# Kernel optimization log

Hardware: AMD Instinct MI355X
Metric: run time of the kernel (lower is better)

The kernel has to match this reference:

```python
import jax, jax.numpy as jnp
import numpy as np

D_MODEL = 192
D_STATE = 16
D_INNER = 384          # expand * d_model
DT_RANK = 12           # ceil(d_model / 16)
K = 4                  # 4 scan directions
B_, H_, W_ = 4, 64, 64
EPS = 1e-6


def setup_inputs() -> dict:
    key = jax.random.key(0)
    ks = jax.random.split(key, 7)
    x = jax.random.normal(ks[0], (B_, H_, W_, D_MODEL), jnp.float32)
    in_proj_weight = jax.random.normal(ks[1], (2 * D_INNER, D_MODEL), jnp.float32) * (D_MODEL ** -0.5)
    out_proj_weight = jax.random.normal(ks[2], (D_MODEL, D_INNER), jnp.float32) * (D_INNER ** -0.5)
    x_proj_weight = jax.random.normal(ks[3], (K, DT_RANK + 2 * D_STATE, D_INNER), jnp.float32) * 0.02
    dt_projs_weight = jax.random.normal(ks[4], (K, D_INNER, DT_RANK), jnp.float32) * (DT_RANK ** -0.5)
    # dt_init: bias = inv_softplus(dt), dt ~ loguniform[1e-3, 1e-1]
    dt = jnp.exp(jax.random.uniform(ks[5], (K, D_INNER)) * (np.log(0.1) - np.log(0.001)) + np.log(0.001))
    dt = jnp.clip(dt, 1e-4, None)
    dt_projs_bias = dt + jnp.log(-jnp.expm1(-dt))
    # A_log_init: log(1..N) repeated over K*d_inner rows
    A_logs = jnp.log(jnp.tile(jnp.arange(1, D_STATE + 1, dtype=jnp.float32)[None, :], (K * D_INNER, 1)))
    Ds = jnp.ones((K * D_INNER,), jnp.float32)
    out_norm_weight = jnp.ones((D_INNER,), jnp.float32)
    out_norm_bias = jnp.zeros((D_INNER,), jnp.float32)
    return dict(x=x, in_proj_weight=in_proj_weight, out_proj_weight=out_proj_weight,
                x_proj_weight=x_proj_weight, dt_projs_weight=dt_projs_weight,
                dt_projs_bias=dt_projs_bias, A_logs=A_logs, Ds=Ds,
                out_norm_weight=out_norm_weight, out_norm_bias=out_norm_bias)


def _selective_scan(u, delta, A, Bs, Cs, Ds, delta_bias):
    """u, delta: (B, K*D, L); A: (K*D, N); Bs, Cs: (B, K, N, L) (grouped); Ds: (K*D,)."""
    Bb, KD, L = u.shape
    N = A.shape[1]
    D = KD // K
    delta = jax.nn.softplus(delta + delta_bias[None, :, None])
    u_k = u.reshape(Bb, K, D, L)
    d_k = delta.reshape(Bb, K, D, L)
    A_k = A.reshape(K, D, N)

    def step(h, inp):
        dt, ut, bt, ct = inp              # dt, ut: (B,K,D); bt, ct: (B,K,N)
        dA = jnp.exp(dt[..., None] * A_k[None])            # (B,K,D,N)
        dBu = dt[..., None] * bt[:, :, None, :] * ut[..., None]
        h = dA * h + dBu
        y = jnp.einsum('bkdn,bkn->bkd', h, ct)
        return h, y

    h0 = jnp.zeros((Bb, K, D, N), u.dtype)
    inps = (jnp.moveaxis(d_k, -1, 0), jnp.moveaxis(u_k, -1, 0),
            jnp.moveaxis(Bs, -1, 0), jnp.moveaxis(Cs, -1, 0))
    _, ys = jax.lax.scan(step, h0, inps)                    # (L, B, K, D)
    y = jnp.moveaxis(ys, 0, -1).reshape(Bb, KD, L)
    return y + u * Ds[None, :, None]


def reference(x, in_proj_weight, out_proj_weight, x_proj_weight, dt_projs_weight,
              dt_projs_bias, A_logs, Ds, out_norm_weight, out_norm_bias):
    Bb, H, W, C = x.shape
    L = H * W
    xz = jnp.einsum('bhwc,ec->bhwe', x, in_proj_weight)     # (B,H,W,2*D_INNER)
    xin, z = jnp.split(xz, 2, axis=-1)
    xc = jnp.transpose(xin, (0, 3, 1, 2))                   # (B,D,H,W)
    x_hw = xc.reshape(Bb, D_INNER, L)
    x_wh = jnp.transpose(xc, (0, 1, 3, 2)).reshape(Bb, D_INNER, L)
    x_hwwh = jnp.stack([x_hw, x_wh], axis=1)                # (B,2,D,L)
    xs = jnp.concatenate([x_hwwh, jnp.flip(x_hwwh, axis=-1)], axis=1)  # (B,4,D,L)

    x_dbl = jnp.einsum('bkdl,kcd->bkcl', xs, x_proj_weight)
    dts = x_dbl[:, :, :DT_RANK]
    Bs = x_dbl[:, :, DT_RANK:DT_RANK + D_STATE]             # (B,4,N,L)
    Cs = x_dbl[:, :, DT_RANK + D_STATE:]
    dts = jnp.einsum('bkrl,kdr->bkdl', dts, dt_projs_weight)

    As = -jnp.exp(A_logs)                                   # (4*D, N)
    out_y = _selective_scan(xs.reshape(Bb, -1, L), dts.reshape(Bb, -1, L), As,
                            Bs, Cs, Ds, dt_projs_bias.reshape(-1)).reshape(Bb, K, D_INNER, L)

    inv_y = jnp.flip(out_y[:, 2:4], axis=-1)                # (B,2,D,L)
    wh_y = jnp.transpose(out_y[:, 1].reshape(Bb, D_INNER, W, H), (0, 1, 3, 2)).reshape(Bb, D_INNER, L)
    invwh_y = jnp.transpose(inv_y[:, 1].reshape(Bb, D_INNER, W, H), (0, 1, 3, 2)).reshape(Bb, D_INNER, L)
    y = out_y[:, 0] + inv_y[:, 0] + wh_y + invwh_y          # (B,D,L)

    # channels_first LayerNorm over channel dim
    y4 = y.reshape(Bb, D_INNER, H, W)
    mu = y4.mean(1, keepdims=True)
    var = ((y4 - mu) ** 2).mean(1, keepdims=True)
    y4 = (y4 - mu) / jnp.sqrt(var + EPS)
    y4 = out_norm_weight[None, :, None, None] * y4 + out_norm_bias[None, :, None, None]

    y = jnp.transpose(y4, (0, 2, 3, 1))                     # (B,H,W,D)
    y = y * jax.nn.silu(z)
    return jnp.einsum('bhwd,cd->bhwc', y, out_proj_weight)
```

## Files before the change

### kernel.cpp

```cpp
#include <hip/hip_runtime.h>

#define L_   4096
#define CM   192
#define DI   384
#define RK   12
#define NS   16
#define CC   44
#define KK   4
#define NCH  64
#define CLEN 64

using bf16x8 = __attribute__((ext_vector_type(8))) short;
using f32x4  = __attribute__((ext_vector_type(4))) float;

__device__ __forceinline__ float dot4acc(float4 a, float4 b, float acc) {
  acc = fmaf(a.x, b.x, acc);
  acc = fmaf(a.y, b.y, acc);
  acc = fmaf(a.z, b.z, acc);
  acc = fmaf(a.w, b.w, acc);
  return acc;
}

__device__ __forceinline__ float fexp2(float x) {
#if __has_builtin(__builtin_amdgcn_exp2f)
  return __builtin_amdgcn_exp2f(x);
#else
  return exp2f(x);
#endif
}

__device__ __forceinline__ unsigned short f2bf(float f) {
  unsigned u = __float_as_uint(f);
  u += 0x7FFFu + ((u >> 16) & 1u);
  return (unsigned short)(u >> 16);
}
__device__ __forceinline__ float bf2f(unsigned short h) {
  return __uint_as_float(((unsigned)h) << 16);
}

#define K1_LDA 72
__global__ __launch_bounds__(256) void k1_inproj(const float* __restrict__ x,
                                                 const float* __restrict__ Win,
                                                 float* __restrict__ xin,
                                                 float* __restrict__ zsil) {
  __shared__ unsigned short Ah[128 * K1_LDA];
  __shared__ unsigned short Al[128 * K1_LDA];
  __shared__ unsigned short Bh[64 * K1_LDA];
  __shared__ unsigned short Bl[64 * K1_LDA];
  const int m0 = blockIdx.x * 128;
  const int n0 = blockIdx.y * 64;
  const int tid = threadIdx.x;
  const int lane = tid & 63;
  const int w = tid >> 6;
  const int wm = w >> 1, wn = w & 1;
  const int l16 = lane & 15;
  const int lk8 = (lane >> 4) * 8;

  f32x4 acc[4][2];
#pragma unroll
  for (int i = 0; i < 4; ++i)
#pragma unroll
    for (int j = 0; j < 2; ++j) acc[i][j] = (f32x4){0.f, 0.f, 0.f, 0.f};

  for (int c = 0; c < 3; ++c) {
    const int kc = c * 64;
#pragma unroll
    for (int it = 0; it < 8; ++it) {
      const int i = tid + it * 256;
      const int row = i >> 4, f4 = i & 15;
      const float4 v = *(const float4*)&x[(size_t)(m0 + row) * CM + kc + f4 * 4];
      ushort4 hi, lo;
      hi.x = f2bf(v.x); lo.x = f2bf(v.x - bf2f(hi.x));
      hi.y = f2bf(v.y); lo.y = f2bf(v.y - bf2f(hi.y));
      hi.z = f2bf(v.z); lo.z = f2bf(v.z - bf2f(hi.z));
      hi.w = f2bf(v.w); lo.w = f2bf(v.w - bf2f(hi.w));
      *(ushort4*)&Ah[row * K1_LDA + f4 * 4] = hi;
      *(ushort4*)&Al[row * K1_LDA + f4 * 4] = lo;
    }
#pragma unroll
    for (int it = 0; it < 4; ++it) {
      const int i = tid + it * 256;
      const int row = i >> 4, f4 = i & 15;
      const float4 v = *(const float4*)&Win[(size_t)(n0 + row) * CM + kc + f4 * 4];
      ushort4 hi, lo;
      hi.x = f2bf(v.x); lo.x = f2bf(v.x - bf2f(hi.x));
      hi.y = f2bf(v.y); lo.y = f2bf(v.y - bf2f(hi.y));
      hi.z = f2bf(v.z); lo.z = f2bf(v.z - bf2f(hi.z));
      hi.w = f2bf(v.w); lo.w = f2bf(v.w - bf2f(hi.w));
      *(ushort4*)&Bh[row * K1_LDA + f4 * 4] = hi;
      *(ushort4*)&Bl[row * K1_LDA + f4 * 4] = lo;
    }
    __syncthreads();
#pragma unroll
    for (int kf = 0; kf < 2; ++kf) {
      const int ko = kf * 32 + lk8;
      bf16x8 ah[4], al[4], bh[2], bl[2];
#pragma unroll
      for (int mi = 0; mi < 4; ++mi) {
        const int r = wm * 64 + mi * 16 + l16;
        ah[mi] = *(const bf16x8*)&Ah[r * K1_LDA + ko];
        al[mi] = *(const bf16x8*)&Al[r * K1_LDA + ko];
      }
#pragma unroll
      for (int ni = 0; ni < 2; ++ni) {
        const int r = wn * 32 + ni * 16 + l16;
        bh[ni] = *(const bf16x8*)&Bh[r * K1_LDA + ko];
        bl[ni] = *(const bf16x8*)&Bl[r * K1_LDA + ko];
      }
#pragma unroll
      for (int mi = 0; mi < 4; ++mi)
#pragma unroll
        for (int ni = 0; ni < 2; ++ni) {
          acc[mi][ni] = __builtin_amdgcn_mfma_f32_16x16x32_bf16(ah[mi], bh[ni], acc[mi][ni], 0, 0, 0);
          acc[mi][ni] = __builtin_amdgcn_mfma_f32_16x16x32_bf16(al[mi], bh[ni], acc[mi][ni], 0, 0, 0);
          acc[mi][ni] = __builtin_amdgcn_mfma_f32_16x16x32_bf16(ah[mi], bl[ni], acc[mi][ni], 0, 0, 0);
        }
    }
    __syncthreads();
  }
#pragma unroll
  for (int mi = 0; mi < 4; ++mi) {
#pragma unroll
    for (int ni = 0; ni < 2; ++ni) {
#pragma unroll
      for (int v = 0; v < 4; ++v) {
        const int row = m0 + wm * 64 + mi * 16 + (lane >> 4) * 4 + v;
        const int col = n0 + wn * 32 + ni * 16 + l16;
        const float val = acc[mi][ni][v];
        if (col < DI) {
          xin[(size_t)row * DI + col] = val;
        } else {
          const float s = 1.f / (1.f + __expf(-val));
          zsil[(size_t)row * DI + (col - DI)] = val * s;
        }
      }
    }
  }
}

#define K2_LDA 72
__global__ __launch_bounds__(256) void k2_xdbl(const float* __restrict__ xin,
                                               const float* __restrict__ Wp,
                                               float* __restrict__ xdbl) {
  __shared__ unsigned short Ah[64 * K2_LDA];
  __shared__ unsigned short Al[64 * K2_LDA];
  __shared__ unsigned short Bh[64 * K2_LDA];
  __shared__ unsigned short Bl[64 * K2_LDA];
  const int m0 = blockIdx.x * 64;
  const int n0 = blockIdx.y * 64;
  const int tid = threadIdx.x;
  const int lane = tid & 63;
  const int w = tid >> 6;
  const int wm = w >> 1, wn = w & 1;
  const int l16 = lane & 15;
  const int lk8 = (lane >> 4) * 8;

  f32x4 acc[2][2];
#pragma unroll
  for (int i = 0; i < 2; ++i)
#pragma unroll
    for (int j = 0; j < 2; ++j) acc[i][j] = (f32x4){0.f, 0.f, 0.f, 0.f};

  for (int c = 0; c < 6; ++c) {
    const int kc = c * 64;
#pragma unroll
    for (int it = 0; it < 4; ++it) {
      const int i = tid + it * 256;
      const int row = i >> 4, f4 = i & 15;
      const float4 v = *(const float4*)&xin[(size_t)(m0 + row) * DI + kc + f4 * 4];
      ushort4 hi, lo;
      hi.x = f2bf(v.x); lo.x = f2bf(v.x - bf2f(hi.x));
      hi.y = f2bf(v.y); lo.y = f2bf(v.y - bf2f(hi.y));
      hi.z = f2bf(v.z); lo.z = f2bf(v.z - bf2f(hi.z));
      hi.w = f2bf(v.w); lo.w = f2bf(v.w - bf2f(hi.w));
      *(ushort4*)&Ah[row * K2_LDA + f4 * 4] = hi;
      *(ushort4*)&Al[row * K2_LDA + f4 * 4] = lo;
    }
#pragma unroll
    for (int it = 0; it < 4; ++it) {
      const int i = tid + it * 256;
      const int row = i >> 4, f4 = i & 15;
      const int gr = n0 + row;
      float4 v = make_float4(0.f, 0.f, 0.f, 0.f);
      if (gr < KK * CC) v = *(const float4*)&Wp[(size_t)gr * DI + kc + f4 * 4];
      ushort4 hi, lo;
      hi.x = f2bf(v.x); lo.x = f2bf(v.x - bf2f(hi.x));
      hi.y = f2bf(v.y); lo.y = f2bf(v.y - bf2f(hi.y));
      hi.z = f2bf(v.z); lo.z = f2bf(v.z - bf2f(hi.z));
      hi.w = f2bf(v.w); lo.w = f2bf(v.w - bf2f(hi.w));
      *(ushort4*)&Bh[row * K2_LDA + f4 * 4] = hi;
      *(ushort4*)&Bl[row * K2_LDA + f4 * 4] = lo;
    }
    __syncthreads();
#pragma unroll
    for (int kf = 0; kf < 2; ++kf) {
      const int ko = kf * 32 + lk8;
      bf16x8 ah[2], al[2], bh[2], bl[2];
#pragma unroll
      for (int mi = 0; mi < 2; ++mi) {
        const int r = wm * 32 + mi * 16 + l16;
        ah[mi] = *(const bf16x8*)&Ah[r * K2_LDA + ko];
        al[mi] = *(const bf16x8*)&Al[r * K2_LDA + ko];
      }
#pragma unroll
      for (int ni = 0; ni < 2; ++ni) {
        const int r = wn * 32 + ni * 16 + l16;
        bh[ni] = *(const bf16x8*)&Bh[r * K2_LDA + ko];
        bl[ni] = *(const bf16x8*)&Bl[r * K2_LDA + ko];
      }
#pragma unroll
      for (int mi = 0; mi < 2; ++mi)
#pragma unroll
        for (int ni = 0; ni < 2; ++ni) {
          acc[mi][ni] = __builtin_amdgcn_mfma_f32_16x16x32_bf16(ah[mi], bh[ni], acc[mi][ni], 0, 0, 0);
          acc[mi][ni] = __builtin_amdgcn_mfma_f32_16x16x32_bf16(al[mi], bh[ni], acc[mi][ni], 0, 0, 0);
          acc[mi][ni] = __builtin_amdgcn_mfma_f32_16x16x32_bf16(ah[mi], bl[ni], acc[mi][ni], 0, 0, 0);
        }
    }
    __syncthreads();
  }
#pragma unroll
  for (int mi = 0; mi < 2; ++mi) {
#pragma unroll
    for (int ni = 0; ni < 2; ++ni) {
#pragma unroll
      for (int v = 0; v < 4; ++v) {
        const int m = m0 + wm * 32 + mi * 16 + (lane >> 4) * 4 + v;
        const int col = n0 + wn * 32 + ni * 16 + l16;
        if (col >= KK * CC) continue;
        const int k = col / CC;
        const int cc = col - k * CC;
        const int b = m >> 12;
        const int pos = m & (L_ - 1);
        const int trp = ((pos & 63) << 6) | (pos >> 6);
        const int js = (k == 0) ? pos : (k == 1) ? trp
                     : (k == 2) ? (L_ - 1 - pos) : (L_ - 1 - trp);
        xdbl[((size_t)(b * KK + k) * L_ + js) * CC + cc] = acc[mi][ni][v];
      }
    }
  }
}

template <int PASS>
__global__ __launch_bounds__(384) void k3_scan(const float* __restrict__ xin,
                                               const float* __restrict__ xdbl,
                                               const float* __restrict__ dtw,
                                               const float* __restrict__ dtb,
                                               const float* __restrict__ Alogs,
                                               const float* __restrict__ Dsv,
                                               const float* __restrict__ hstart,
                                               float* __restrict__ summH,
                                               float* __restrict__ summS,
                                               float* __restrict__ ysum) {
  __shared__ float xd[CLEN][CC];
  const int blk = blockIdx.x;
  const int ch = blk & (NCH - 1);
  const int bk = blk >> 6;
  const int k = bk & 3, b = bk >> 2;
  const int d = threadIdx.x;
  const int j0 = ch * CLEN;

  {
    const float4* src = (const float4*)(xdbl + ((size_t)bk * L_ + j0) * CC);
    float4* dst = (float4*)&xd[0][0];
    for (int i = d; i < CLEN * CC / 4; i += 384) dst[i] = src[i];
  }

  const int kd = k * DI + d;
  const float c0 = -__expf(Alogs[(size_t)kd * NS]) * 1.442695041f;
  float h[NS];
#pragma unroll
  for (int n = 0; n < NS; ++n) h[n] = 0.f;
  if (PASS == 1) {
    const float4* hs = (const float4*)(hstart + ((size_t)blk * DI + d) * NS);
    float4 h0 = hs[0], h1 = hs[1], h2 = hs[2], h3 = hs[3];
    h[0] = h0.x; h[1] = h0.y; h[2] = h0.z; h[3] = h0.w;
    h[4] = h1.x; h[5] = h1.y; h[6] = h1.z; h[7] = h1.w;
    h[8] = h2.x; h[9] = h2.y; h[10] = h2.z; h[11] = h2.w;
    h[12] = h3.x; h[13] = h3.y; h[14] = h3.z; h[15] = h3.w;
  }
  float4 w0, w1, w2;
  {
    const float4* w4 = (const float4*)(dtw + (size_t)kd * RK);
    w0 = w4[0]; w1 = w4[1]; w2 = w4[2];
  }
  const float bias = dtb[kd];
  const float Dk = (PASS == 1) ? Dsv[kd] : 0.f;
  __syncthreads();

  float Sdt = 0.f;
#pragma unroll 2
  for (int t = 0; t < CLEN; ++t) {
    const int j = j0 + t;
    int pos;
    if (k == 0) pos = j;
    else if (k == 1) pos = ((j & 63) << 6) | (j >> 6);
    else if (k == 2) pos = L_ - 1 - j;
    else { const int jj = L_ - 1 - j; pos = ((jj & 63) << 6) | (jj >> 6); }

    const float u = xin[((size_t)b * L_ + pos) * DI + d];
    const float4* row4 = (const float4*)xd[t];
    float4 q0 = row4[0], q1 = row4[1], q2 = row4[2];
    float dtv = bias;
    dtv = dot4acc(q0, w0, dtv);
    dtv = dot4acc(q1, w1, dtv);
    dtv = dot4acc(q2, w2, dtv);
    dtv = (dtv > 20.f) ? dtv : __logf(1.f + __expf(dtv));

    float bb[NS];
    *(float4*)&bb[0] = row4[3];
    *(float4*)&bb[4] = row4[4];
    *(float4*)&bb[8] = row4[5];
    *(float4*)&bb[12] = row4[6];
    const float du = dtv * u;

    const float e1 = fexp2(dtv * c0);
    const float e2 = e1 * e1;
    const float e4 = e2 * e2;
    const float e8 = e4 * e4;
    float dA[NS];
    dA[0] = e1;       dA[1] = e2;       dA[2] = e2 * e1;   dA[3] = e4;
    dA[4] = e4 * e1;  dA[5] = e4 * e2;  dA[6] = e4 * dA[2]; dA[7] = e8;
    dA[8] = e8 * e1;  dA[9] = e8 * e2;  dA[10] = e8 * dA[2]; dA[11] = e8 * e4;
    dA[12] = e8 * dA[4]; dA[13] = e8 * dA[5]; dA[14] = e8 * dA[6]; dA[15] = e8 * e8;
#pragma unroll
    for (int n = 0; n < NS; ++n) h[n] = fmaf(dA[n], h[n], bb[n] * du);

    if (PASS == 0) {
      Sdt += dtv;
    } else {
      float cc[NS];
      *(float4*)&cc[0] = row4[7];
      *(float4*)&cc[4] = row4[8];
      *(float4*)&cc[8] = row4[9];
      *(float4*)&cc[12] = row4[10];
      float y0 = 0.f, y1 = 0.f, y2 = 0.f, y3 = 0.f;
#pragma unroll
      for (int n = 0; n < 4; ++n) {
        y0 = fmaf(h[n], cc[n], y0);
        y1 = fmaf(h[4 + n], cc[4 + n], y1);
        y2 = fmaf(h[8 + n], cc[8 + n], y2);
        y3 = fmaf(h[12 + n], cc[12 + n], y3);
      }
      float y = (y0 + y1) + (y2 + y3);
      y = fmaf(u, Dk, y);
      atomicAdd(&ysum[((size_t)b * L_ + pos) * DI + d], y);
    }
  }

  if (PASS == 0) {
    float4* o = (float4*)(summH + ((size_t)blk * DI + d) * NS);
    o[0] = make_float4(h[0], h[1], h[2], h[3]);
    o[1] = make_float4(h[4], h[5], h[6], h[7]);
    o[2] = make_float4(h[8], h[9], h[10], h[11]);
    o[3] = make_float4(h[12], h[13], h[14], h[15]);
    summS[(size_t)blk * DI + d] = Sdt;
  }
}

__global__ __launch_bounds__(256) void k3_stitch(const float* __restrict__ Alogs,
                                                 const float* __restrict__ summH,
                                                 const float* __restrict__ summS,
                                                 float* __restrict__ hstart) {
  const int t = blockIdx.x * 256 + threadIdx.x;
  const int n = t & 15;
  const int rd = t >> 4;
  const int bk = rd / DI;
  const int d = rd - bk * DI;
  const int k = bk & 3;
  const int kd = k * DI + d;
  const float A2 = -__expf(Alogs[(size_t)kd * NS + n]) * 1.442695041f;
  float h = 0.f;
  for (int c = 0; c < NCH; ++c) {
    const size_t base = (size_t)(bk * NCH + c) * DI + d;
    hstart[base * NS + n] = h;
    const float S = summS[base];
    h = fmaf(fexp2(A2 * S), h, summH[base * NS + n]);
  }
}

#define K4_LDA 72
__global__ __launch_bounds__(256) void k4_out(const float* __restrict__ ysum,
                                              const float* __restrict__ zsil,
                                              const float* __restrict__ wln,
                                              const float* __restrict__ bln,
                                              const float* __restrict__ Wout,
                                              float* __restrict__ out) {
  __shared__ unsigned short Ah[64 * K4_LDA];
  __shared__ unsigned short Al[64 * K4_LDA];
  __shared__ unsigned short Bh[64 * K4_LDA];
  __shared__ unsigned short Bl[64 * K4_LDA];
  __shared__ float smu[64], srs[64];
  const int m0 = blockIdx.x * 64;
  const int n0 = blockIdx.y * 64;
  const int tid = threadIdx.x;
  const int lane = tid & 63;
  const int w = tid >> 6;
  const int wm = w >> 1, wn = w & 1;
  const int l16 = lane & 15;
  const int lk8 = (lane >> 4) * 8;

  {
    const int row = tid >> 2, q = tid & 3;
    const float4* p = (const float4*)&ysum[(size_t)(m0 + row) * DI + q * 96];
    float s1 = 0.f, s2 = 0.f;
#pragma unroll
    for (int i = 0; i < 24; ++i) {
      const float4 v = p[i];
      s1 += v.x + v.y + v.z + v.w;
      s2 = fmaf(v.x, v.x, s2);
      s2 = fmaf(v.y, v.y, s2);
      s2 = fmaf(v.z, v.z, s2);
      s2 = fmaf(v.w, v.w, s2);
    }
    s1 += __shfl_xor(s1, 1);
    s2 += __shfl_xor(s2, 1);
    s1 += __shfl_xor(s1, 2);
    s2 += __shfl_xor(s2, 2);
    if (q == 0) {
      const float mu = s1 * (1.f / DI);
      const float var = s2 * (1.f / DI) - mu * mu;
      smu[row] = mu;
      srs[row] = rsqrtf(var + 1e-6f);
    }
  }
  __syncthreads();

  f32x4 acc[2][2];
#pragma unroll
  for (int i = 0; i < 2; ++i)
#pragma unroll
    for (int j = 0; j < 2; ++j) acc[i][j] = (f32x4){0.f, 0.f, 0.f, 0.f};

  for (int c = 0; c < 6; ++c) {
    const int kc = c * 64;
#pragma unroll
    for (int it = 0; it < 4; ++it) {
      const int i = tid + it * 256;
      const int row = i >> 4, f4 = i & 15;
      const float mu = smu[row], rs = srs[row];
      const float4 v = *(const float4*)&ysum[(size_t)(m0 + row) * DI + kc + f4 * 4];
      const float4 z = *(const float4*)&zsil[(size_t)(m0 + row) * DI + kc + f4 * 4];
      const float4 wl = *(const float4*)&wln[kc + f4 * 4];
      const float4 bl = *(const float4*)&bln[kc + f4 * 4];
      float4 g;
      g.x = fmaf((v.x - mu) * rs, wl.x, bl.x) * z.x;
      g.y = fmaf((v.y - mu) * rs, wl.y, bl.y) * z.y;
      g.z = fmaf((v.z - mu) * rs, wl.z, bl.z) * z.z;
      g.w = fmaf((v.w - mu) * rs, wl.w, bl.w) * z.w;
      ushort4 hi, lo;
      hi.x = f2bf(g.x); lo.x = f2bf(g.x - bf2f(hi.x));
      hi.y = f2bf(g.y); lo.y = f2bf(g.y - bf2f(hi.y));
      hi.z = f2bf(g.z); lo.z = f2bf(g.z - bf2f(hi.z));
      hi.w = f2bf(g.w); lo.w = f2bf(g.w - bf2f(hi.w));
      *(ushort4*)&Ah[row * K4_LDA + f4 * 4] = hi;
      *(ushort4*)&Al[row * K4_LDA + f4 * 4] = lo;
    }
#pragma unroll
    for (int it = 0; it < 4; ++it) {
      const int i = tid + it * 256;
      const int row = i >> 4, f4 = i & 15;
      const float4 v = *(const float4*)&Wout[(size_t)(n0 + row) * DI + kc + f4 * 4];
      ushort4 hi, lo;
      hi.x = f2bf(v.x); lo.x = f2bf(v.x - bf2f(hi.x));
      hi.y = f2bf(v.y); lo.y = f2bf(v.y - bf2f(hi.y));
      hi.z = f2bf(v.z); lo.z = f2bf(v.z - bf2f(hi.z));
      hi.w = f2bf(v.w); lo.w = f2bf(v.w - bf2f(hi.w));
      *(ushort4*)&Bh[row * K4_LDA + f4 * 4] = hi;
      *(ushort4*)&Bl[row * K4_LDA + f4 * 4] = lo;
    }
    __syncthreads();
#pragma unroll
    for (int kf = 0; kf < 2; ++kf) {
      const int ko = kf * 32 + lk8;
      bf16x8 ah[2], al[2], bh[2], bl[2];
#pragma unroll
      for (int mi = 0; mi < 2; ++mi) {
        const int r = wm * 32 + mi * 16 + l16;
        ah[mi] = *(const bf16x8*)&Ah[r * K4_LDA + ko];
        al[mi] = *(const bf16x8*)&Al[r * K4_LDA + ko];
      }
#pragma unroll
      for (int ni = 0; ni < 2; ++ni) {
        const int r = wn * 32 + ni * 16 + l16;
        bh[ni] = *(const bf16x8*)&Bh[r * K4_LDA + ko];
        bl[ni] = *(const bf16x8*)&Bl[r * K4_LDA + ko];
      }
#pragma unroll
      for (int mi = 0; mi < 2; ++mi)
#pragma unroll
        for (int ni = 0; ni < 2; ++ni) {
          acc[mi][ni] = __builtin_amdgcn_mfma_f32_16x16x32_bf16(ah[mi], bh[ni], acc[mi][ni], 0, 0, 0);
          acc[mi][ni] = __builtin_amdgcn_mfma_f32_16x16x32_bf16(al[mi], bh[ni], acc[mi][ni], 0, 0, 0);
          acc[mi][ni] = __builtin_amdgcn_mfma_f32_16x16x32_bf16(ah[mi], bl[ni], acc[mi][ni], 0, 0, 0);
        }
    }
    __syncthreads();
  }
#pragma unroll
  for (int mi = 0; mi < 2; ++mi) {
#pragma unroll
    for (int ni = 0; ni < 2; ++ni) {
#pragma unroll
      for (int v = 0; v < 4; ++v) {
        const int row = m0 + wm * 32 + mi * 16 + (lane >> 4) * 4 + v;
        const int col = n0 + wn * 32 + ni * 16 + l16;
        out[(size_t)row * CM + col] = acc[mi][ni][v];
      }
    }
  }
}

extern "C" void kernel_launch(void* const* d_in, const int* in_sizes, int n_in,
                              void* d_out, int out_size, void* d_ws, size_t ws_size,
                              hipStream_t stream) {
  (void)in_sizes; (void)n_in; (void)out_size; (void)ws_size;
  const float* x    = (const float*)d_in[0];
  const float* Win  = (const float*)d_in[1];
  const float* Wout = (const float*)d_in[2];
  const float* Wp   = (const float*)d_in[3];
  const float* dtw  = (const float*)d_in[4];
  const float* dtb  = (const float*)d_in[5];
  const float* Alog = (const float*)d_in[6];
  const float* Ds   = (const float*)d_in[7];
  const float* wln  = (const float*)d_in[8];
  const float* bln  = (const float*)d_in[9];
  float* out = (float*)d_out;

  float* ws     = (float*)d_ws;
  float* xin    = ws;
  float* zsil   = xin + 6291456;
  float* xdbl   = zsil + 6291456;
  float* summH  = xdbl + 2883584;
  float* summS  = summH + 6291456;
  float* hstart = summS + 393216;
  float* ysum   = summH;

  k1_inproj<<<dim3(128, 12), 256, 0, stream>>>(x, Win, xin, zsil);
  k2_xdbl<<<dim3(256, 3), 256, 0, stream>>>(xin, Wp, xdbl);
  k3_scan<0><<<1024, 384, 0, stream>>>(xin, xdbl, dtw, dtb, Alog, Ds, nullptr,
                                       summH, summS, nullptr);
  k3_stitch<<<384, 256, 0, stream>>>(Alog, summH, summS, hstart);
  hipMemsetAsync(ysum, 0, (size_t)6291456 * sizeof(float), stream);
  k3_scan<1><<<1024, 384, 0, stream>>>(xin, xdbl, dtw, dtb, Alog, Ds, hstart,
                                       nullptr, nullptr, ysum);
  k4_out<<<dim3(256, 3), 256, 0, stream>>>(ysum, zsil, wln, bln, Wout, out);
}
```

Measured before the change: 250.3 us.

## Replace two-pass chunked scan with forward pass plus closed-form carry-in correction

The first scan pass now also emits per-chunk outputs from a zero initial state and stores cumulative dt per step in fp16. A light correction kernel then adds C·(h_start ⊙ exp(A·cumdt)), so the scan recurrence and dt projection are not recomputed in a second full pass. The correction costs an extra write and read of the cumdt buffer, more workspace, and fp16 rounding of cumdt, which may reduce accuracy. If the workspace is too small, it falls back to the old path.

```diff
diff --git a/kernel.cpp b/kernel.cpp
--- a/kernel.cpp
+++ b/kernel.cpp
@@ -355,6 +355,188 @@
     o[2] = make_float4(h[8], h[9], h[10], h[11]);
     o[3] = make_float4(h[12], h[13], h[14], h[15]);
     summS[(size_t)blk * DI + d] = Sdt;
+  }
+}
+
+__global__ __launch_bounds__(384) void k3_fwd(const float* __restrict__ xin,
+                                              const float* __restrict__ xdbl,
+                                              const float* __restrict__ dtw,
+                                              const float* __restrict__ dtb,
+                                              const float* __restrict__ Alogs,
+                                              const float* __restrict__ Dsv,
+                                              float* __restrict__ summH,
+                                              float* __restrict__ summS,
+                                              _Float16* __restrict__ cums,
+                                              float* __restrict__ ysum) {
+  __shared__ float xd[CLEN][CC];
+  const int blk = blockIdx.x;
+  const int ch = blk & (NCH - 1);
+  const int bk = blk >> 6;
+  const int k = bk & 3, b = bk >> 2;
+  const int d = threadIdx.x;
+  const int j0 = ch * CLEN;
+
+  {
+    const float4* src = (const float4*)(xdbl + ((size_t)bk * L_ + j0) * CC);
+    float4* dst = (float4*)&xd[0][0];
+    for (int i = d; i < CLEN * CC / 4; i += 384) dst[i] = src[i];
+  }
+
+  const int kd = k * DI + d;
+  const float c0 = -__expf(Alogs[(size_t)kd * NS]) * 1.442695041f;
+  float h[NS];
+#pragma unroll
+  for (int n = 0; n < NS; ++n) h[n] = 0.f;
+  float4 w0, w1, w2;
+  {
+    const float4* w4 = (const float4*)(dtw + (size_t)kd * RK);
+    w0 = w4[0]; w1 = w4[1]; w2 = w4[2];
+  }
+  const float bias = dtb[kd];
+  const float Dk = Dsv[kd];
+  __syncthreads();
+
+  float cumdt = 0.f;
+#pragma unroll 2
+  for (int t = 0; t < CLEN; ++t) {
+    const int j = j0 + t;
+    int pos;
+    if (k == 0) pos = j;
+    else if (k == 1) pos = ((j & 63) << 6) | (j >> 6);
+    else if (k == 2) pos = L_ - 1 - j;
+    else { const int jj = L_ - 1 - j; pos = ((jj & 63) << 6) | (jj >> 6); }
+
+    const float u = xin[((size_t)b * L_ + pos) * DI + d];
+    const float4* row4 = (const float4*)xd[t];
+    float4 q0 = row4[0], q1 = row4[1], q2 = row4[2];
+    float dtv = bias;
+    dtv = dot4acc(q0, w0, dtv);
+    dtv = dot4acc(q1, w1, dtv);
+    dtv = dot4acc(q2, w2, dtv);
+    dtv = (dtv > 20.f) ? dtv : __logf(1.f + __expf(dtv));
+
+    cumdt += dtv;
+    cums[((size_t)blk * CLEN + t) * DI + d] = (_Float16)cumdt;
+
+    float bb[NS];
+    *(float4*)&bb[0] = row4[3];
+    *(float4*)&bb[4] = row4[4];
+    *(float4*)&bb[8] = row4[5];
+    *(float4*)&bb[12] = row4[6];
+    const float du = dtv * u;
+
+    const float e1 = fexp2(dtv * c0);
+    const float e2 = e1 * e1;
+    const float e4 = e2 * e2;
+    const float e8 = e4 * e4;
+    float dA[NS];
+    dA[0] = e1;       dA[1] = e2;       dA[2] = e2 * e1;   dA[3] = e4;
+    dA[4] = e4 * e1;  dA[5] = e4 * e2;  dA[6] = e4 * dA[2]; dA[7] = e8;
+    dA[8] = e8 * e1;  dA[9] = e8 * e2;  dA[10] = e8 * dA[2]; dA[11] = e8 * e4;
+    dA[12] = e8 * dA[4]; dA[13] = e8 * dA[5]; dA[14] = e8 * dA[6]; dA[15] = e8 * e8;
+#pragma unroll
+    for (int n = 0; n < NS; ++n) h[n] = fmaf(dA[n], h[n], bb[n] * du);
+
+    float cc[NS];
+    *(float4*)&cc[0] = row4[7];
+    *(float4*)&cc[4] = row4[8];
+    *(float4*)&cc[8] = row4[9];
+    *(float4*)&cc[12] = row4[10];
+    float y0 = 0.f, y1 = 0.f, y2 = 0.f, y3 = 0.f;
+#pragma unroll
+    for (int n = 0; n < 4; ++n) {
+      y0 = fmaf(h[n], cc[n], y0);
+      y1 = fmaf(h[4 + n], cc[4 + n], y1);
+      y2 = fmaf(h[8 + n], cc[8 + n], y2);
+      y3 = fmaf(h[12 + n], cc[12 + n], y3);
+    }
+    float y = (y0 + y1) + (y2 + y3);
+    y = fmaf(u, Dk, y);
+    atomicAdd(&ysum[((size_t)b * L_ + pos) * DI + d], y);
+  }
+
+  float4* o = (float4*)(summH + ((size_t)blk * DI + d) * NS);
+  o[0] = make_float4(h[0], h[1], h[2], h[3]);
+  o[1] = make_float4(h[4], h[5], h[6], h[7]);
+  o[2] = make_float4(h[8], h[9], h[10], h[11]);
+  o[3] = make_float4(h[12], h[13], h[14], h[15]);
+  summS[(size_t)blk * DI + d] = cumdt;
+}
+
+__global__ __launch_bounds__(384) void k3_corr(const float* __restrict__ xdbl,
+                                               const float* __restrict__ Alogs,
+                                               const float* __restrict__ hstart,
+                                               const _Float16* __restrict__ cums,
+                                               float* __restrict__ ysum) {
+  __shared__ float xd[CLEN][CC];
+  const int blk = blockIdx.x;
+  const int ch = blk & (NCH - 1);
+  const int bk = blk >> 6;
+  const int k = bk & 3, b = bk >> 2;
+  const int d = threadIdx.x;
+  const int j0 = ch * CLEN;
+
+  {
+    const float4* src = (const float4*)(xdbl + ((size_t)bk * L_ + j0) * CC);
+    float4* dst = (float4*)&xd[0][0];
+    for (int i = d; i < CLEN * CC / 4; i += 384) dst[i] = src[i];
+  }
+
+  const int kd = k * DI + d;
+  const float c0 = -__expf(Alogs[(size_t)kd * NS]) * 1.442695041f;
+  float h0[NS];
+  {
+    const float4* hs = (const float4*)(hstart + ((size_t)blk * DI + d) * NS);
+    float4 a = hs[0], bq = hs[1], cq = hs[2], dq = hs[3];
+    h0[0] = a.x;  h0[1] = a.y;  h0[2] = a.z;  h0[3] = a.w;
+    h0[4] = bq.x; h0[5] = bq.y; h0[6] = bq.z; h0[7] = bq.w;
+    h0[8] = cq.x; h0[9] = cq.y; h0[10] = cq.z; h0[11] = cq.w;
+    h0[12] = dq.x; h0[13] = dq.y; h0[14] = dq.z; h0[15] = dq.w;
+  }
+  __syncthreads();
+
+  float az = 0.f;
+#pragma unroll
+  for (int n = 0; n < NS; ++n) az += fabsf(h0[n]);
+  if (az == 0.f) return;
+
+#pragma unroll 2
+  for (int t = 0; t < CLEN; ++t) {
+    const int j = j0 + t;
+    int pos;
+    if (k == 0) pos = j;
+    else if (k == 1) pos = ((j & 63) << 6) | (j >> 6);
+    else if (k == 2) pos = L_ - 1 - j;
+    else { const int jj = L_ - 1 - j; pos = ((jj & 63) << 6) | (jj >> 6); }
+
+    const float cumdt = (float)cums[((size_t)blk * CLEN + t) * DI + d];
+    const float e1 = fexp2(cumdt * c0);
+    const float e2 = e1 * e1;
+    const float e4 = e2 * e2;
+    const float e8 = e4 * e4;
+    float P[NS];
+    P[0] = e1;       P[1] = e2;       P[2] = e2 * e1;   P[3] = e4;
+    P[4] = e4 * e1;  P[5] = e4 * e2;  P[6] = e4 * P[2]; P[7] = e8;
+    P[8] = e8 * e1;  P[9] = e8 * e2;  P[10] = e8 * P[2]; P[11] = e8 * e4;
+    P[12] = e8 * P[4]; P[13] = e8 * P[5]; P[14] = e8 * P[6]; P[15] = e8 * e8;
+
+    const float4* row4 = (const float4*)xd[t];
+    float cc[NS];
+    *(float4*)&cc[0] = row4[7];
+    *(float4*)&cc[4] = row4[8];
+    *(float4*)&cc[8] = row4[9];
+    *(float4*)&cc[12] = row4[10];
+
+    float y0 = 0.f, y1 = 0.f, y2 = 0.f, y3 = 0.f;
+#pragma unroll
+    for (int n = 0; n < 4; ++n) {
+      y0 = fmaf(h0[n] * P[n], cc[n], y0);
+      y1 = fmaf(h0[4 + n] * P[4 + n], cc[4 + n], y1);
+      y2 = fmaf(h0[8 + n] * P[8 + n], cc[8 + n], y2);
+      y3 = fmaf(h0[12 + n] * P[12 + n], cc[12 + n], y3);
+    }
+    const float corr = (y0 + y1) + (y2 + y3);
+    atomicAdd(&ysum[((size_t)b * L_ + pos) * DI + d], corr);
   }
 }
 
@@ -514,7 +696,7 @@
 extern "C" void kernel_launch(void* const* d_in, const int* in_sizes, int n_in,
                               void* d_out, int out_size, void* d_ws, size_t ws_size,
                               hipStream_t stream) {
-  (void)in_sizes; (void)n_in; (void)out_size; (void)ws_size;
+  (void)in_sizes; (void)n_in; (void)out_size;
   const float* x    = (const float*)d_in[0];
   const float* Win  = (const float*)d_in[1];
   const float* Wout = (const float*)d_in[2];
@@ -527,22 +709,45 @@
   const float* bln  = (const float*)d_in[9];
   float* out = (float*)d_out;
 
-  float* ws     = (float*)d_ws;
-  float* xin    = ws;
-  float* zsil   = xin + 6291456;
-  float* xdbl   = zsil + 6291456;
-  float* summH  = xdbl + 2883584;
-  float* summS  = summH + 6291456;
-  float* hstart = summS + 393216;
-  float* ysum   = summH;
-
-  k1_inproj<<<dim3(128, 12), 256, 0, stream>>>(x, Win, xin, zsil);
-  k2_xdbl<<<dim3(256, 3), 256, 0, stream>>>(xin, Wp, xdbl);
-  k3_scan<0><<<1024, 384, 0, stream>>>(xin, xdbl, dtw, dtb, Alog, Ds, nullptr,
-                                       summH, summS, nullptr);
-  k3_stitch<<<384, 256, 0, stream>>>(Alog, summH, summS, hstart);
-  hipMemsetAsync(ysum, 0, (size_t)6291456 * sizeof(float), stream);
-  k3_scan<1><<<1024, 384, 0, stream>>>(xin, xdbl, dtw, dtb, Alog, Ds, hstart,
-                                       nullptr, nullptr, ysum);
-  k4_out<<<dim3(256, 3), 256, 0, stream>>>(ysum, zsil, wln, bln, Wout, out);
-}
+  float* ws = (float*)d_ws;
+  const size_t NEED = (size_t)34734080 * 4 + (size_t)25165824 * 2;
+
+  k1_inproj<<<dim3(128, 12), 256, 0, stream>>>(x, Win, ws ,
+                                               ws + 6291456 );
+
+  if (ws_size >= NEED) {
+    float* xin    = ws;
+    float* zsil   = xin + 6291456;
+    float* xdbl   = zsil + 6291456;
+    float* summH  = xdbl + 2883584;
+    float* summS  = summH + 6291456;
+    float* hstart = summS + 393216;
+    float* ysum   = hstart + 6291456;
+    _Float16* cums = (_Float16*)(ysum + 6291456);
+
+    k2_xdbl<<<dim3(256, 3), 256, 0, stream>>>(xin, Wp, xdbl);
+    hipMemsetAsync(ysum, 0, (size_t)6291456 * sizeof(float), stream);
+    k3_fwd<<<1024, 384, 0, stream>>>(xin, xdbl, dtw, dtb, Alog, Ds,
+                                     summH, summS, cums, ysum);
+    k3_stitch<<<384, 256, 0, stream>>>(Alog, summH, summS, hstart);
+    k3_corr<<<1024, 384, 0, stream>>>(xdbl, Alog, hstart, cums, ysum);
+    k4_out<<<dim3(256, 3), 256, 0, stream>>>(ysum, zsil, wln, bln, Wout, out);
+  } else {
+    float* xin    = ws;
+    float* zsil   = xin + 6291456;
+    float* xdbl   = zsil + 6291456;
+    float* summH  = xdbl + 2883584;
+    float* summS  = summH + 6291456;
+    float* hstart = summS + 393216;
+    float* ysum   = summH;
+
+    k2_xdbl<<<dim3(256, 3), 256, 0, stream>>>(xin, Wp, xdbl);
+    k3_scan<0><<<1024, 384, 0, stream>>>(xin, xdbl, dtw, dtb, Alog, Ds, nullptr,
+                                         summH, summS, nullptr);
+    k3_stitch<<<384, 256, 0, stream>>>(Alog, summH, summS, hstart);
+    hipMemsetAsync(ysum, 0, (size_t)6291456 * sizeof(float), stream);
+    k3_scan<1><<<1024, 384, 0, stream>>>(xin, xdbl, dtw, dtb, Alog, Ds, hstart,
+                                         nullptr, nullptr, ysum);
+    k4_out<<<dim3(256, 3), 256, 0, stream>>>(ysum, zsil, wln, bln, Wout, out);
+  }
+}
```

After: 276.7 us. +10.6%, slower.
